# Performance work log

Measured on AMD Instinct MI355X. Metric: run time of the kernel, lower is better.

## Reference

```python
import jax, jax.numpy as jnp
import numpy as np

TAU = 2.0       # LIF time constant
ALPHA = 4.0     # spikingjelly Sigmoid surrogate alpha
EPS = 1e-5      # BatchNorm eps
NUM_HEADS = 8

@jax.custom_vjp
def _spike(x):
    return (x >= 0.0).astype(x.dtype)

def _spike_fwd(x):
    return _spike(x), x

def _spike_bwd(x, g):
    s = jax.nn.sigmoid(ALPHA * x)
    return (g * ALPHA * s * (1.0 - s),)

_spike.defvjp(_spike_fwd, _spike_bwd)

def lif(x, v_th=1.0):
    """Multi-step LIF over leading time axis. v <- v + (x - v)/tau; hard reset to 0.
    detach_reset=True: spike in reset path is stop-gradient'ed."""
    def step(v, xt):
        v = v + (xt - v) / TAU
        s = _spike(v - v_th)
        v = v * (1.0 - jax.lax.stop_gradient(s))
        return v, s
    _, out = jax.lax.scan(step, jnp.zeros_like(x[0]), x)
    return out

def conv_bn(x, w, gamma, beta, mean, var, bias=None):
    """1x1 Conv1d over channel dim + BatchNorm1d (inference-style, running stats).
    x: [T,B,C,N], w: [Cout,Cin]."""
    y = jnp.einsum('tbcn,dc->tbdn', x, w)
    if bias is not None:
        y = y + bias[None, None, :, None]
    inv = gamma * jax.lax.rsqrt(var + EPS)
    return (y - mean[None, None, :, None]) * inv[None, None, :, None] + beta[None, None, :, None]

def _bn_params(key, C):
    k1, k2, k3 = jax.random.split(key, 3)
    gamma = 1.0 + 0.1 * jax.random.normal(k1, (C,), jnp.float32)
    beta = 0.1 * jax.random.normal(k2, (C,), jnp.float32)
    mean = 0.1 * jax.random.normal(k3, (C,), jnp.float32)
    var = jnp.ones((C,), jnp.float32)
    return gamma, beta, mean, var

def setup_inputs() -> dict:
    key = jax.random.key(0)
    ks = jax.random.split(key, 10)
    T, B, C, N = 4, 8, 512, 1024
    scale = 1.0 / np.sqrt(C)
    d = {}
    d['q'] = jax.random.normal(ks[0], (T, B, C, N), jnp.float32)
    d['k'] = jax.random.normal(ks[1], (T, B, C, N), jnp.float32)
    d['q_w'] = jax.random.normal(ks[2], (C, C), jnp.float32) * scale
    d['k_w'] = jax.random.normal(ks[3], (C, C), jnp.float32) * scale
    d['proj_w'] = jax.random.normal(ks[4], (C, C), jnp.float32) * scale
    d['proj_b'] = 0.01 * jax.random.normal(ks[5], (C,), jnp.float32)
    d['q_gamma'], d['q_beta'], d['q_mean'], d['q_var'] = _bn_params(ks[6], C)
    d['k_gamma'], d['k_beta'], d['k_mean'], d['k_var'] = _bn_params(ks[7], C)
    d['proj_gamma'], d['proj_beta'], d['proj_mean'], d['proj_var'] = _bn_params(ks[8], C)
    return d

def reference(q, k, q_w, k_w, proj_w, proj_b,
              q_gamma, q_beta, q_mean, q_var,
              k_gamma, k_beta, k_mean, k_var,
              proj_gamma, proj_beta, proj_mean, proj_var):
    T, B, C, N = q.shape
    H = NUM_HEADS
    Dh = C // H
    # Q path: conv1x1 + BN + LIF spikes, split heads
    q_s = lif(conv_bn(q, q_w, q_gamma, q_beta, q_mean, q_var))          # [T,B,C,N]
    q_h = q_s.reshape(T, B, H, Dh, N)
    # K path
    k_s = lif(conv_bn(k, k_w, k_gamma, k_beta, k_mean, k_var))          # [T,B,C,N]
    k_h = k_s.reshape(T, B, H, Dh, N)
    # Sum-pool Q over head_dim, spike-gate (threshold 0.5), multiply into K
    q_sum = jnp.sum(q_h, axis=3, keepdims=True)                         # [T,B,H,1,N]
    attn = lif(q_sum, v_th=0.5)                                         # [T,B,H,1,N]
    x = (attn * k_h).reshape(T, B, C, N)
    # Projection: conv1x1 (with bias) + BN + LIF
    x = conv_bn(x, proj_w, proj_gamma, proj_beta, proj_mean, proj_var, bias=proj_b)
    return lif(x)
```

## Files before the change

kernel.cpp:

```cpp
#include <hip/hip_runtime.h>
#include <hip/hip_fp16.h>
#include <stdint.h>

#define TT 4
#define BB 8
#define CC 512
#define NN 1024
#define HH 8

typedef unsigned char u8;
typedef _Float16 f16x8 __attribute__((ext_vector_type(8)));
typedef float f32x16 __attribute__((ext_vector_type(16)));

#define WF_BYTES ((size_t)2*64*512*16)
#define SZ_SPIKE ((size_t)TT*BB*CC*NN)
#define SZ_GATE  ((size_t)TT*BB*HH*NN)

union U4H { uint4 u; f16x8 v; };
__device__ __forceinline__ f16x8 ash(uint4 u){ U4H x; x.u = u; return x.v; }

#define MFMA_F16(a,b,c) __builtin_amdgcn_mfma_f32_32x32x16_f16((a),(b),(c),0,0,0)

__device__ __forceinline__ void gld_lds4(const void* g, void* l){
  __builtin_amdgcn_global_load_lds((const __attribute__((address_space(1))) void*)g,
                                   (__attribute__((address_space(3))) void*)l, 4, 0, 0);
}

#define WAITVM(N) asm volatile("s_waitcnt vmcnt(" #N ")" ::: "memory")
#define WAITLGKM0 asm volatile("s_waitcnt lgkmcnt(0)" ::: "memory")
#define SBAR() __builtin_amdgcn_s_barrier()
#define VMFENCE() asm volatile("" ::: "memory")

__device__ __forceinline__ void split16(float xs, uint32_t& h, uint32_t& m){
  __half hh = __float2half(xs);
  float hf = __half2float(hh);
  __half mm = __float2half(xs - hf);
  h = __half_as_ushort(hh);
  m = __half_as_ushort(mm);
}

__global__ __launch_bounds__(256)
void k_prep(const float* __restrict__ W0, const float* __restrict__ W1,
            const float* __restrict__ W2,
            u8* __restrict__ D0, u8* __restrict__ D1, u8* __restrict__ D2)
{
  const int which = blockIdx.y;
  const float* W = (which == 0) ? W0 : (which == 1) ? W1 : W2;
  u8* D = (which == 0) ? D0 : (which == 1) ? D1 : D2;
  const int tg  = blockIdx.x * 256 + threadIdx.x;
  const int row = tg >> 6;
  const int kh  = tg & 63;
  uint32_t Hw[4], Mw[4];
#pragma unroll
  for (int p = 0; p < 4; ++p){
    uint32_t h0, m0, h1, m1;
    split16(W[row * CC + kh * 8 + 2*p    ] * 64.0f, h0, m0);
    split16(W[row * CC + kh * 8 + 2*p + 1] * 64.0f, h1, m1);
    Hw[p] = h0 | (h1 << 16);
    Mw[p] = m0 | (m1 << 16);
  }
  *(uint4*)(D + ((size_t)(0*64 + kh)*512 + row) * 16) = make_uint4(Hw[0],Hw[1],Hw[2],Hw[3]);
  *(uint4*)(D + ((size_t)(1*64 + kh)*512 + row) * 16) = make_uint4(Mw[0],Mw[1],Mw[2],Mw[3]);
}

__global__ __launch_bounds__(256, 2)
void k_qk(const float* __restrict__ Q, const float* __restrict__ K,
          const u8* __restrict__ WFq, const u8* __restrict__ WFk,
          const float* __restrict__ qg, const float* __restrict__ qb,
          const float* __restrict__ qm, const float* __restrict__ qv,
          const float* __restrict__ kg, const float* __restrict__ kb,
          const float* __restrict__ km, const float* __restrict__ kv,
          u8* __restrict__ Sk, u8* __restrict__ Aa)
{
  __shared__ uint4 frag[2][1024];

  const int hw = blockIdx.x;
  const int lg = (hw & 7) * 128 + (hw >> 3);
  const int d0t  = lg & 1;
  const int n0i  = (lg >> 1) & 31;
  const int b    = (lg >> 6) & 7;
  const int path = (lg >> 9) & 1;
  const int n0 = n0i << 5, d0 = d0t << 8;
  const float* X = path ? K : Q;
  const u8* WF = path ? WFk : WFq;

  const int tid = threadIdx.x, lane = tid & 63, wid = tid >> 6;
  const int hi = lane >> 5, ln31 = lane & 31;

  const int c  = tid & 127;
  const int kq = tid >> 7;
  const int ct_t = c >> 5, nn = c & 31;
  const float* Xb = X + ((size_t)(ct_t*BB + b)*CC)*NN + n0 + nn;

  f32x16 acc[4][2];
#pragma unroll
  for (int i = 0; i < 4; ++i)
#pragma unroll
    for (int j = 0; j < 2; ++j)
#pragma unroll
      for (int r = 0; r < 16; ++r) acc[i][j][r] = 0.0f;

  uint4 A[8];
  float xb[2][16];

  auto loadA = [&](int H){
#pragma unroll
    for (int s = 0; s < 2; ++s)
#pragma unroll
      for (int ks = 0; ks < 2; ++ks)
#pragma unroll
        for (int rt = 0; rt < 2; ++rt)
          A[(s*2 + ks)*2 + rt] = *(const uint4*)(WF +
              ((size_t)(s*64 + H*4 + ks*2 + hi)*512
               + d0 + wid*64 + rt*32 + ln31) * 16);
  };
  auto loadX = [&](int ktile, float* xr){
    const float* xp = Xb + (size_t)(ktile*32 + kq*16)*NN;
#pragma unroll
    for (int j = 0; j < 16; ++j) xr[j] = xp[(size_t)j*NN];
  };
  auto split_write = [&](const float* xr, int fb){
    uint32_t hw_[8], mw_[8];
#pragma unroll
    for (int p = 0; p < 8; ++p){
      uint32_t ha, ma, hb2, mb2;
      split16(xr[2*p    ] * 512.0f, ha, ma);
      split16(xr[2*p + 1] * 512.0f, hb2, mb2);
      hw_[p] = ha | (hb2 << 16);
      mw_[p] = ma | (mb2 << 16);
    }
    frag[fb][(kq*2    )*128 + c] = make_uint4(hw_[0],hw_[1],hw_[2],hw_[3]);
    frag[fb][(kq*2 + 1)*128 + c] = make_uint4(hw_[4],hw_[5],hw_[6],hw_[7]);
    frag[fb][(4 + kq*2    )*128 + c] = make_uint4(mw_[0],mw_[1],mw_[2],mw_[3]);
    frag[fb][(4 + kq*2 + 1)*128 + c] = make_uint4(mw_[4],mw_[5],mw_[6],mw_[7]);
  };
  auto mstep = [&](int fb){
#pragma unroll
    for (int ks = 0; ks < 2; ++ks){
      const int kbi = ks*2 + hi;
#pragma unroll
      for (int ct = 0; ct < 4; ++ct){
        f16x8 bh = ash(frag[fb][kbi*128 + ct*32 + ln31]);
        f16x8 bm = ash(frag[fb][(4 + kbi)*128 + ct*32 + ln31]);
#pragma unroll
        for (int rt = 0; rt < 2; ++rt){
          acc[ct][rt] = MFMA_F16(ash(A[(0*2 + ks)*2 + rt]), bh, acc[ct][rt]);
          acc[ct][rt] = MFMA_F16(ash(A[(1*2 + ks)*2 + rt]), bh, acc[ct][rt]);
          acc[ct][rt] = MFMA_F16(ash(A[(0*2 + ks)*2 + rt]), bm, acc[ct][rt]);
        }
      }
    }
  };

#define QK_PH(H, XL, XN, FC, FN) { \
    loadA(H); VMFENCE(); \
    loadX((H)+2, xb[XN]); VMFENCE(); \
    split_write(xb[XL], FN); \
    mstep(FC); \
    WAITLGKM0; SBAR(); }

  loadX(0, xb[0]); VMFENCE();
  loadX(1, xb[1]); VMFENCE();
  split_write(xb[0], 0);
  WAITLGKM0; SBAR();

  for (int Hb = 0; Hb < 14; Hb += 2){
    QK_PH(Hb,     1, 0, 0, 1)
    QK_PH(Hb + 1, 0, 1, 1, 0)
  }
  { loadA(14); VMFENCE(); split_write(xb[1], 1); mstep(0); WAITLGKM0; SBAR(); }
  { loadA(15); VMFENCE(); mstep(1); }
#undef QK_PH

  const float* gamma = path ? kg : qg;
  const float* beta  = path ? kb : qb;
  const float* mean  = path ? km : qm;
  const float* var   = path ? kv : qv;

  uint32_t orb = 0;
#pragma unroll
  for (int rt = 0; rt < 2; ++rt)
#pragma unroll
    for (int rg = 0; rg < 4; ++rg){
      const int dbase = d0 + wid*64 + rt*32 + rg*8 + hi*4;
      const float4 g4 = *(const float4*)&gamma[dbase];
      const float4 b4 = *(const float4*)&beta[dbase];
      const float4 m4 = *(const float4*)&mean[dbase];
      const float4 v4 = *(const float4*)&var[dbase];
      const float* gp = (const float*)&g4;
      const float* bp = (const float*)&b4;
      const float* mp = (const float*)&m4;
      const float* vp = (const float*)&v4;
#pragma unroll
      for (int j = 0; j < 4; ++j){
        const float inv = gp[j] * (1.0f / sqrtf(vp[j] + 1e-5f));
        const float c1 = inv * (1.0f/32768.0f);
        const float c0 = bp[j] - mp[j]*inv;
        const int r = rg*4 + j;
        float v = 0.f;
#pragma unroll
        for (int t = 0; t < 4; ++t){
          const float y = fmaf(acc[t][rt][r], c1, c0);
          v = 0.5f*(v + y);
          const bool s = (v >= 1.0f);
          if (s) v = 0.f;
          if (path == 1)
            Sk[((size_t)(t*BB + b)*CC + dbase + j)*NN + n0 + ln31] = (u8)s;
          else
            orb |= ((uint32_t)s) << t;
        }
      }
    }

  if (path == 0){
    orb |= __shfl_xor(orb, 32);
    if (hi == 0){
      const int h = d0t*4 + wid;
#pragma unroll
      for (int t = 0; t < 4; ++t)
        Aa[((size_t)(t*BB + b)*HH + h)*NN + n0 + ln31] = (u8)((orb >> t) & 1);
    }
  }
}

__global__ __launch_bounds__(256, 2)
void k_proj(const u8* __restrict__ Sk, const u8* __restrict__ Ag,
            const u8* __restrict__ WF, const float* __restrict__ bias,
            const float* __restrict__ gamma, const float* __restrict__ beta,
            const float* __restrict__ mean, const float* __restrict__ var,
            float* __restrict__ O)
{
  __shared__ u8   xu[3][8192];
  __shared__ uint4 frag[1024];

  const int hw = blockIdx.x;
  const int lg = (hw & 7) * 64 + (hw >> 3);
  const int d0t = lg & 1;
  const int n0i = (lg >> 1) & 31;
  const int b   = (lg >> 6) & 7;
  const int n0 = n0i << 5, d0 = d0t << 8;

  const int tid = threadIdx.x, lane = tid & 63, wid = tid >> 6;
  const int hi = lane >> 5, ln31 = lane & 31;

  const int st_kh = tid >> 5, st_t = (tid >> 3) & 3, st_n4 = tid & 7;

  f32x16 acc[4][2];
#pragma unroll
  for (int t = 0; t < 4; ++t)
#pragma unroll
    for (int rt = 0; rt < 2; ++rt)
#pragma unroll
      for (int r = 0; r < 16; ++r) acc[t][rt][r] = 0.0f;

  uint4 Ap[16];
  uint32_t gword[8];
#pragma unroll
  for (int p = 0; p < 8; ++p)
    gword[p] = *(const uint32_t*)(Ag +
        ((size_t)(st_t*BB + b)*HH + p)*NN + n0 + st_n4*4);

  auto xustage = [&](int h, int buf){
#pragma unroll
    for (int i = 0; i < 8; ++i){
      const u8* g = Sk + ((size_t)((wid*BB + b)*CC) + (size_t)(h*64 + i*8 + (lane >> 3)))*NN
                       + n0 + (lane & 7)*4;
      gld_lds4(g, (void*)&xu[buf][(wid*64 + i*8)*32]);
    }
  };
  auto loadPA = [&](int p){
#pragma unroll
    for (int s = 0; s < 2; ++s)
#pragma unroll
      for (int ks = 0; ks < 4; ++ks)
#pragma unroll
        for (int rt = 0; rt < 2; ++rt)
          Ap[(s*4 + ks)*2 + rt] = *(const uint4*)(WF +
              ((size_t)(s*64 + p*8 + ks*2 + hi)*512
               + d0 + wid*64 + rt*32 + ln31) * 16);
  };
  auto stage2 = [&](int buf, uint32_t g32){
    uint32_t r[8];
#pragma unroll
    for (int cc = 0; cc < 8; ++cc)
      r[cc] = *(const uint32_t*)&xu[buf][(st_t*64 + st_kh*8 + cc)*32 + st_n4*4];
#pragma unroll
    for (int j = 0; j < 4; ++j){
      const uint32_t gm   = __builtin_amdgcn_perm(g32, g32, (uint32_t)j * 0x01010101u);
      const uint32_t selp = (uint32_t)j | (((uint32_t)j + 4u) << 8);
      uint32_t p01 = __builtin_amdgcn_perm(r[1], r[0], selp);
      uint32_t p23 = __builtin_amdgcn_perm(r[3], r[2], selp);
      uint32_t p45 = __builtin_amdgcn_perm(r[5], r[4], selp);
      uint32_t p67 = __builtin_amdgcn_perm(r[7], r[6], selp);
      uint32_t lo  = __builtin_amdgcn_perm(p23, p01, 0x05040100u) & gm;
      uint32_t hi_ = __builtin_amdgcn_perm(p67, p45, 0x05040100u) & gm;
      uint32_t w[4];
#pragma unroll
      for (int p = 0; p < 4; ++p){
        const uint32_t src = (p < 2) ? lo : hi_;
        const uint32_t b0 = (src >> ((p & 1) * 16)) & 0xFFu;
        const uint32_t b1 = (src >> ((p & 1) * 16 + 8)) & 0xFFu;
        w[p] = (b0 ? 0x3C00u : 0u) | (b1 ? 0x3C000000u : 0u);
      }
      frag[st_kh*128 + st_t*32 + st_n4*4 + j] = make_uint4(w[0], w[1], w[2], w[3]);
    }
  };
  auto mstepP = [&](){
#pragma unroll
    for (int ks = 0; ks < 4; ++ks){
      const int kbi = ks*2 + hi;
#pragma unroll
      for (int ct = 0; ct < 4; ++ct){
        const int fb = ct*32 + ln31;
        f16x8 bb = ash(frag[kbi*128 + fb]);
#pragma unroll
        for (int rt = 0; rt < 2; ++rt){
          acc[ct][rt] = MFMA_F16(ash(Ap[(0*4 + ks)*2 + rt]), bb, acc[ct][rt]);
          acc[ct][rt] = MFMA_F16(ash(Ap[(1*4 + ks)*2 + rt]), bb, acc[ct][rt]);
        }
      }
    }
  };

#define PJ_PH(P, VM) { \
    WAITVM(VM); SBAR(); \
    loadPA(P); VMFENCE(); \
    if ((P) < 6) { xustage((P)+2, ((P)+2)%3); VMFENCE(); } \
    stage2((P)%3, gword[P]); \
    WAITLGKM0; SBAR(); \
    mstepP(); }

  xustage(0, 0); VMFENCE(); xustage(1, 1); VMFENCE();
  PJ_PH(0,8) PJ_PH(1,8) PJ_PH(2,8) PJ_PH(3,8)
  PJ_PH(4,8) PJ_PH(5,8) PJ_PH(6,8) PJ_PH(7,0)
#undef PJ_PH

#pragma unroll
  for (int rt = 0; rt < 2; ++rt)
#pragma unroll
    for (int rg = 0; rg < 4; ++rg){
      const int dbase = d0 + wid*64 + rt*32 + rg*8 + hi*4;
      const float4 g4 = *(const float4*)&gamma[dbase];
      const float4 b4 = *(const float4*)&beta[dbase];
      const float4 m4 = *(const float4*)&mean[dbase];
      const float4 v4 = *(const float4*)&var[dbase];
      const float4 s4 = *(const float4*)&bias[dbase];
      const float* gp = (const float*)&g4;
      const float* bp = (const float*)&b4;
      const float* mp = (const float*)&m4;
      const float* vp = (const float*)&v4;
      const float* sp = (const float*)&s4;
#pragma unroll
      for (int j = 0; j < 4; ++j){
        const float inv = gp[j] * (1.0f / sqrtf(vp[j] + 1e-5f));
        const float c1 = inv * (1.0f/64.0f);
        const float c0 = (sp[j] - mp[j])*inv + bp[j];
        const int r = rg*4 + j;
        float v = 0.f;
#pragma unroll
        for (int t = 0; t < 4; ++t){
          const float y = fmaf(acc[t][rt][r], c1, c0);
          v = 0.5f*(v + y);
          const bool s = (v >= 1.0f);
          if (s) v = 0.f;
          O[((size_t)(t*BB + b)*CC + dbase + j)*NN + n0 + ln31] = s ? 1.f : 0.f;
        }
      }
    }
}

extern "C" void kernel_launch(void* const* d_in, const int* in_sizes, int n_in,
                              void* d_out, int out_size, void* d_ws, size_t ws_size,
                              hipStream_t stream)
{
  const float* q   = (const float*)d_in[0];
  const float* k   = (const float*)d_in[1];
  const float* qw  = (const float*)d_in[2];
  const float* kw  = (const float*)d_in[3];
  const float* pw  = (const float*)d_in[4];
  const float* pb  = (const float*)d_in[5];
  const float* qg  = (const float*)d_in[6];
  const float* qbt = (const float*)d_in[7];
  const float* qm  = (const float*)d_in[8];
  const float* qv  = (const float*)d_in[9];
  const float* kg  = (const float*)d_in[10];
  const float* kbt = (const float*)d_in[11];
  const float* km  = (const float*)d_in[12];
  const float* kv  = (const float*)d_in[13];
  const float* pg  = (const float*)d_in[14];
  const float* pbt = (const float*)d_in[15];
  const float* pm  = (const float*)d_in[16];
  const float* pv  = (const float*)d_in[17];

  u8* WFq = (u8*)d_ws;
  u8* WFk = WFq + WF_BYTES;
  u8* WFp = WFk + WF_BYTES;
  u8* Sk  = WFp + WF_BYTES;
  u8* Aa  = Sk + SZ_SPIKE;
  const size_t need = 3*WF_BYTES + SZ_SPIKE + SZ_GATE;
  if (ws_size < need) return;

  k_prep<<<dim3(128, 3), 256, 0, stream>>>(qw, kw, pw, WFq, WFk, WFp);
  k_qk<<<1024, 256, 0, stream>>>(q, k, WFq, WFk,
                                 qg, qbt, qm, qv, kg, kbt, km, kv, Sk, Aa);
  k_proj<<<512, 256, 0, stream>>>(Sk, Aa, WFp, pb, pg, pbt, pm, pv, (float*)d_out);
}
```

Measured before the change: 164.2 us.

## Cover all 512 output channels per k_qk block with 512 threads and double-buffered weights

k_qk now launches 512 blocks of 512 threads, and each block computes the full 512-row output-channel dimension instead of half. The activation tile is converted and staged once for all channels, which removes the duplicate X loads and hi/mid split work that the two d0 halves used to repeat. Weight fragments are double-buffered in registers (A0/A1) and partial vmcnt waits let the next loads overlap the MFMA steps. In exchange the block is larger and register pressure rises, which may cut occupancy, and the code relies on the unshown Xb/kq indexing lining up with 512 threads.

New measurement: 158.8 us. 3.3% less time.

```diff
diff --git a/kernel.cpp b/kernel.cpp
--- a/kernel.cpp
+++ b/kernel.cpp
@@ -63,7 +63,7 @@
   *(uint4*)(D + ((size_t)(1*64 + kh)*512 + row) * 16) = make_uint4(Mw[0],Mw[1],Mw[2],Mw[3]);
 }
 
-__global__ __launch_bounds__(256, 2)
+__global__ __launch_bounds__(512, 2)
 void k_qk(const float* __restrict__ Q, const float* __restrict__ K,
           const u8* __restrict__ WFq, const u8* __restrict__ WFk,
           const float* __restrict__ qg, const float* __restrict__ qb,
@@ -75,12 +75,11 @@
   __shared__ uint4 frag[2][1024];
 
   const int hw = blockIdx.x;
-  const int lg = (hw & 7) * 128 + (hw >> 3);
-  const int d0t  = lg & 1;
-  const int n0i  = (lg >> 1) & 31;
-  const int b    = (lg >> 6) & 7;
-  const int path = (lg >> 9) & 1;
-  const int n0 = n0i << 5, d0 = d0t << 8;
+  const int lg = (hw & 7) * 64 + (hw >> 3);
+  const int n0i  = lg & 31;
+  const int b    = (lg >> 5) & 7;
+  const int path = (lg >> 8) & 1;
+  const int n0 = n0i << 5;
   const float* X = path ? K : Q;
   const u8* WF = path ? WFk : WFq;
 
@@ -100,77 +99,82 @@
 #pragma unroll
       for (int r = 0; r < 16; ++r) acc[i][j][r] = 0.0f;
 
-  uint4 A[8];
-  float xb[2][16];
-
-  auto loadA = [&](int H){
+  uint4 A0[8], A1[8];
+  float xr[8];
+
+  auto loadX = [&](int tile){
+    const float* xp = Xb + (size_t)(tile*32 + kq*8)*NN;
+#pragma unroll
+    for (int j = 0; j < 8; ++j) xr[j] = xp[(size_t)j*NN];
+  };
+  auto loadA = [&](int H, uint4* A){
 #pragma unroll
     for (int s = 0; s < 2; ++s)
 #pragma unroll
-      for (int ks = 0; ks < 2; ++ks)
+      for (int ksc = 0; ksc < 2; ++ksc)
 #pragma unroll
         for (int rt = 0; rt < 2; ++rt)
-          A[(s*2 + ks)*2 + rt] = *(const uint4*)(WF +
-              ((size_t)(s*64 + H*4 + ks*2 + hi)*512
-               + d0 + wid*64 + rt*32 + ln31) * 16);
-  };
-  auto loadX = [&](int ktile, float* xr){
-    const float* xp = Xb + (size_t)(ktile*32 + kq*16)*NN;
-#pragma unroll
-    for (int j = 0; j < 16; ++j) xr[j] = xp[(size_t)j*NN];
-  };
-  auto split_write = [&](const float* xr, int fb){
-    uint32_t hw_[8], mw_[8];
-#pragma unroll
-    for (int p = 0; p < 8; ++p){
+          A[(s*2 + ksc)*2 + rt] = *(const uint4*)(WF +
+              ((size_t)(s*64 + H*4 + ksc*2 + hi)*512
+               + wid*64 + rt*32 + ln31) * 16);
+  };
+  auto split_write = [&](int fb){
+    uint32_t hw_[4], mw_[4];
+#pragma unroll
+    for (int p = 0; p < 4; ++p){
       uint32_t ha, ma, hb2, mb2;
       split16(xr[2*p    ] * 512.0f, ha, ma);
       split16(xr[2*p + 1] * 512.0f, hb2, mb2);
       hw_[p] = ha | (hb2 << 16);
       mw_[p] = ma | (mb2 << 16);
     }
-    frag[fb][(kq*2    )*128 + c] = make_uint4(hw_[0],hw_[1],hw_[2],hw_[3]);
-    frag[fb][(kq*2 + 1)*128 + c] = make_uint4(hw_[4],hw_[5],hw_[6],hw_[7]);
-    frag[fb][(4 + kq*2    )*128 + c] = make_uint4(mw_[0],mw_[1],mw_[2],mw_[3]);
-    frag[fb][(4 + kq*2 + 1)*128 + c] = make_uint4(mw_[4],mw_[5],mw_[6],mw_[7]);
-  };
-  auto mstep = [&](int fb){
-#pragma unroll
-    for (int ks = 0; ks < 2; ++ks){
-      const int kbi = ks*2 + hi;
+    frag[fb][      kq*128 + c] = make_uint4(hw_[0],hw_[1],hw_[2],hw_[3]);
+    frag[fb][(4 + kq)*128 + c] = make_uint4(mw_[0],mw_[1],mw_[2],mw_[3]);
+  };
+  auto mstep = [&](const uint4* A, int fb){
+#pragma unroll
+    for (int ksc = 0; ksc < 2; ++ksc){
+      const int klr = ksc*2 + hi;
 #pragma unroll
       for (int ct = 0; ct < 4; ++ct){
-        f16x8 bh = ash(frag[fb][kbi*128 + ct*32 + ln31]);
-        f16x8 bm = ash(frag[fb][(4 + kbi)*128 + ct*32 + ln31]);
+        f16x8 bh = ash(frag[fb][klr*128 + ct*32 + ln31]);
+        f16x8 bm = ash(frag[fb][(4 + klr)*128 + ct*32 + ln31]);
 #pragma unroll
         for (int rt = 0; rt < 2; ++rt){
-          acc[ct][rt] = MFMA_F16(ash(A[(0*2 + ks)*2 + rt]), bh, acc[ct][rt]);
-          acc[ct][rt] = MFMA_F16(ash(A[(1*2 + ks)*2 + rt]), bh, acc[ct][rt]);
-          acc[ct][rt] = MFMA_F16(ash(A[(0*2 + ks)*2 + rt]), bm, acc[ct][rt]);
+          acc[ct][rt] = MFMA_F16(ash(A[(0*2 + ksc)*2 + rt]), bh, acc[ct][rt]);
+          acc[ct][rt] = MFMA_F16(ash(A[(1*2 + ksc)*2 + rt]), bh, acc[ct][rt]);
+          acc[ct][rt] = MFMA_F16(ash(A[(0*2 + ksc)*2 + rt]), bm, acc[ct][rt]);
         }
       }
     }
   };
 
-#define QK_PH(H, XL, XN, FC, FN) { \
-    loadA(H); VMFENCE(); \
-    loadX((H)+2, xb[XN]); VMFENCE(); \
-    split_write(xb[XL], FN); \
-    mstep(FC); \
+  loadX(0); VMFENCE();
+  loadA(0, A0); VMFENCE();
+  WAITVM(8);
+  split_write(0);
+  loadX(1); VMFENCE();
+  WAITLGKM0; SBAR();
+
+#define QK_IT(H, AC, AN) { \
+    loadA((H)+1, AN); VMFENCE(); \
+    WAITVM(16); \
+    mstep(AC, (H)&1); \
+    WAITVM(8); \
+    split_write(((H)+1)&1); \
+    if ((H) < 14) { loadX((H)+2); VMFENCE(); } \
     WAITLGKM0; SBAR(); }
 
-  loadX(0, xb[0]); VMFENCE();
-  loadX(1, xb[1]); VMFENCE();
-  split_write(xb[0], 0);
-  WAITLGKM0; SBAR();
-
-  for (int Hb = 0; Hb < 14; Hb += 2){
-    QK_PH(Hb,     1, 0, 0, 1)
-    QK_PH(Hb + 1, 0, 1, 1, 0)
-  }
-  { loadA(14); VMFENCE(); split_write(xb[1], 1); mstep(0); WAITLGKM0; SBAR(); }
-  { loadA(15); VMFENCE(); mstep(1); }
-#undef QK_PH
+  QK_IT(0,  A0, A1)  QK_IT(1,  A1, A0)
+  QK_IT(2,  A0, A1)  QK_IT(3,  A1, A0)
+  QK_IT(4,  A0, A1)  QK_IT(5,  A1, A0)
+  QK_IT(6,  A0, A1)  QK_IT(7,  A1, A0)
+  QK_IT(8,  A0, A1)  QK_IT(9,  A1, A0)
+  QK_IT(10, A0, A1)  QK_IT(11, A1, A0)
+  QK_IT(12, A0, A1)  QK_IT(13, A1, A0)
+  QK_IT(14, A0, A1)
+  { WAITVM(0); mstep(A1, 1); }
+#undef QK_IT
 
   const float* gamma = path ? kg : qg;
   const float* beta  = path ? kb : qb;
@@ -182,7 +186,7 @@
   for (int rt = 0; rt < 2; ++rt)
 #pragma unroll
     for (int rg = 0; rg < 4; ++rg){
-      const int dbase = d0 + wid*64 + rt*32 + rg*8 + hi*4;
+      const int dbase = wid*64 + rt*32 + rg*8 + hi*4;
       const float4 g4 = *(const float4*)&gamma[dbase];
       const float4 b4 = *(const float4*)&beta[dbase];
       const float4 m4 = *(const float4*)&mean[dbase];
@@ -215,10 +219,9 @@
   if (path == 0){
     orb |= __shfl_xor(orb, 32);
     if (hi == 0){
-      const int h = d0t*4 + wid;
 #pragma unroll
       for (int t = 0; t < 4; ++t)
-        Aa[((size_t)(t*BB + b)*HH + h)*NN + n0 + ln31] = (u8)((orb >> t) & 1);
+        Aa[((size_t)(t*BB + b)*HH + wid)*NN + n0 + ln31] = (u8)((orb >> t) & 1);
     }
   }
 }
@@ -401,7 +404,7 @@
   if (ws_size < need) return;
 
   k_prep<<<dim3(128, 3), 256, 0, stream>>>(qw, kw, pw, WFq, WFk, WFp);
-  k_qk<<<1024, 256, 0, stream>>>(q, k, WFq, WFk,
-                                 qg, qbt, qm, qv, kg, kbt, km, kv, Sk, Aa);
+  k_qk<<<512, 512, 0, stream>>>(q, k, WFq, WFk,
+                                qg, qbt, qm, qv, kg, kbt, km, kv, Sk, Aa);
   k_proj<<<512, 256, 0, stream>>>(Sk, Aa, WFp, pb, pg, pbt, pm, pv, (float*)d_out);
 }
```
